# Performance work log

Measured on AMD Instinct MI355X. Metric: run time of the kernel, lower is better.

## Reference

```python
import jax, jax.numpy as jnp
import numpy as np
from jax import lax

D_MODEL = 1024
D_STATE = 16
D_CONV = 4
EXPAND = 2
D_INNER = EXPAND * D_MODEL           # 2048 (mamba inner)
DT_RANK = (D_MODEL + 15) // 16       # 64
D_FF = 4 * D_MODEL                   # 4096 (SwiGLU hidden)
EPS = 1e-5
B, L = 2, 2048


def setup_inputs() -> dict:
    key = jax.random.key(0)
    ks = jax.random.split(key, 16)
    s = 0.02
    inp = {
        'x': jax.random.normal(ks[0], (B, L, D_MODEL), jnp.float32),
        'norm1_w': jnp.ones((D_MODEL,), jnp.float32),
        'norm2_w': jnp.ones((D_MODEL,), jnp.float32),
        # Mamba params (torch Linear convention: y = x @ W.T)
        'in_proj_w': s * jax.random.normal(ks[1], (2 * D_INNER, D_MODEL), jnp.float32),
        'conv_w': s * jax.random.normal(ks[2], (D_INNER, 1, D_CONV), jnp.float32),
        'conv_b': jnp.zeros((D_INNER,), jnp.float32),
        'x_proj_w': s * jax.random.normal(ks[3], (DT_RANK + 2 * D_STATE, D_INNER), jnp.float32),
        'dt_proj_w': s * jax.random.normal(ks[4], (D_INNER, DT_RANK), jnp.float32),
        'dt_proj_b': jax.random.uniform(ks[5], (D_INNER,), jnp.float32, -4.0, -2.0),
        'A_log': jnp.log(jnp.broadcast_to(jnp.arange(1, D_STATE + 1, dtype=jnp.float32), (D_INNER, D_STATE))),
        'D': jnp.ones((D_INNER,), jnp.float32),
        'out_proj_w': s * jax.random.normal(ks[6], (D_MODEL, D_INNER), jnp.float32),
        # SwiGLU MLP
        'w1': s * jax.random.normal(ks[7], (D_FF, D_MODEL), jnp.float32),
        'w2': s * jax.random.normal(ks[8], (D_FF, D_MODEL), jnp.float32),
        'w3': s * jax.random.normal(ks[9], (D_MODEL, D_FF), jnp.float32),
    }
    return inp


def _rmsnorm(x, w, eps=EPS):
    return x * lax.rsqrt(jnp.mean(x * x, axis=-1, keepdims=True) + eps) * w


def _mamba(x, in_proj_w, conv_w, conv_b, x_proj_w, dt_proj_w, dt_proj_b, A_log, Dp, out_proj_w):
    # x: (B, L, d_model)
    xz = x @ in_proj_w.T                       # (B, L, 2*d_inner)
    u, z = jnp.split(xz, 2, axis=-1)           # each (B, L, d_inner)
    # causal depthwise conv1d over time
    u_nch = u.transpose(0, 2, 1)               # (B, d_inner, L)
    u_conv = lax.conv_general_dilated(
        u_nch, conv_w, window_strides=(1,), padding=[(D_CONV - 1, 0)],
        dimension_numbers=('NCH', 'OIH', 'NCH'), feature_group_count=D_INNER)
    u_conv = u_conv + conv_b[None, :, None]
    u_act = jax.nn.silu(u_conv.transpose(0, 2, 1))   # (B, L, d_inner)
    # input-dependent dt, B, C
    proj = u_act @ x_proj_w.T                  # (B, L, dt_rank + 2*d_state)
    dt_r, Bm, Cm = jnp.split(proj, [DT_RANK, DT_RANK + D_STATE], axis=-1)
    dt = jax.nn.softplus(dt_r @ dt_proj_w.T + dt_proj_b)   # (B, L, d_inner)
    A = -jnp.exp(A_log)                        # (d_inner, d_state)
    dA = jnp.exp(jnp.einsum('bld,dn->bldn', dt, A))
    dBu = jnp.einsum('bld,bln,bld->bldn', dt, Bm, u_act)
    def step(h, inputs):
        dA_t, dBu_t = inputs                   # (B, d_inner, d_state)
        h = dA_t * h + dBu_t
        return h, h
    h0 = jnp.zeros((x.shape[0], D_INNER, D_STATE), x.dtype)
    _, hs = lax.scan(step, h0, (dA.transpose(1, 0, 2, 3), dBu.transpose(1, 0, 2, 3)))
    y = jnp.einsum('lbdn,bln->bld', hs, Cm) + u_act * Dp   # (B, L, d_inner)
    y = y * jax.nn.silu(z)
    return y @ out_proj_w.T                    # (B, L, d_model)


def reference(x, norm1_w, norm2_w, in_proj_w, conv_w, conv_b, x_proj_w,
              dt_proj_w, dt_proj_b, A_log, D, out_proj_w, w1, w2, w3):
    # residual + RMSNorm + Mamba (dropout = eval-mode identity)
    h = x + _mamba(_rmsnorm(x, norm1_w), in_proj_w, conv_w, conv_b,
                   x_proj_w, dt_proj_w, dt_proj_b, A_log, D, out_proj_w)
    # residual + RMSNorm + SwiGLU MLP
    xn = _rmsnorm(h, norm2_w)
    mlp = (jax.nn.silu(xn @ w1.T) * (xn @ w2.T)) @ w3.T
    return h + mlp
```

## Files before the change

kernel.cpp:

```cpp
#include <hip/hip_runtime.h>
#include <hip/hip_bf16.h>

#define TOKS 4096
#define DM   1024
#define DI   2048
#define DST  16
#define DTR  64
#define DFF  4096
#define PROJ_LD 128

#define NC    32
#define CHUNK 64

typedef __bf16 bf16x8 __attribute__((ext_vector_type(8)));
typedef float  f32x4  __attribute__((ext_vector_type(4)));

__device__ __forceinline__ __bf16 f2bf(float f) {
  union { float f; unsigned u; } v; v.f = f;
  unsigned r = v.u + 0x7fffu + ((v.u >> 16) & 1u);
  union { unsigned short s; __bf16 b; } o; o.s = (unsigned short)(r >> 16);
  return o.b;
}
__device__ __forceinline__ float siluf(float x) { return x / (1.f + __expf(-x)); }
__device__ __forceinline__ float softplusf(float x) { return x > 20.f ? x : log1pf(__expf(x)); }

__device__ __forceinline__ void gl2lds16(const void* g, void* l) {
  __builtin_amdgcn_global_load_lds((const __attribute__((address_space(1))) void*)g,
                                   (__attribute__((address_space(3))) void*)l, 16, 0, 0);
}

struct CvtArgs {
  const float* src[5];
  __bf16*      dst[5];
  int nblk[6];
};

__global__ __launch_bounds__(256) void cvt_bf16_kernel(CvtArgs a) {
  int blk = blockIdx.x;
  int seg = 0;
#pragma unroll
  for (int s = 1; s < 5; s++) if (blk >= a.nblk[s]) seg = s;
  size_t base = (size_t)(blk - a.nblk[seg]) * 2048 + threadIdx.x * 8;
  const float* src = a.src[seg] + base;
  __bf16*      dst = a.dst[seg] + base;
  float4 v0 = *(const float4*)src;
  float4 v1 = *(const float4*)(src + 4);
  union { __bf16 b[8]; uint4 u; } t;
  t.b[0]=f2bf(v0.x); t.b[1]=f2bf(v0.y); t.b[2]=f2bf(v0.z); t.b[3]=f2bf(v0.w);
  t.b[4]=f2bf(v1.x); t.b[5]=f2bf(v1.y); t.b[6]=f2bf(v1.z); t.b[7]=f2bf(v1.w);
  *(uint4*)dst = t.u;
}

__global__ __launch_bounds__(256) void cvt_w12_kernel(const float* __restrict__ w1,
                                                      const float* __restrict__ w2,
                                                      __bf16* __restrict__ dst) {
  int blk = blockIdx.x;
  int isw2 = blk >> 11;
  int b = blk & 2047;
  int r = b * 2 + (threadIdx.x >> 7);
  int col = (threadIdx.x & 127) * 8;
  const float* src = (isw2 ? w2 : w1) + (size_t)r * DM + col;
  int dr = (r >> 4) * 32 + (r & 15) + isw2 * 16;
  float4 v0 = *(const float4*)src;
  float4 v1 = *(const float4*)(src + 4);
  union { __bf16 b[8]; uint4 u; } t;
  t.b[0]=f2bf(v0.x); t.b[1]=f2bf(v0.y); t.b[2]=f2bf(v0.z); t.b[3]=f2bf(v0.w);
  t.b[4]=f2bf(v1.x); t.b[5]=f2bf(v1.y); t.b[6]=f2bf(v1.z); t.b[7]=f2bf(v1.w);
  *(uint4*)&dst[(size_t)dr * DM + col] = t.u;
}

__global__ __launch_bounds__(256) void rmsnorm_kernel(const float* __restrict__ x,
                                                      const float* __restrict__ w,
                                                      __bf16* __restrict__ out) {
  int row = blockIdx.x;
  const float* xr = x + (size_t)row * DM;
  float4 v = ((const float4*)xr)[threadIdx.x];
  float ss = v.x*v.x + v.y*v.y + v.z*v.z + v.w*v.w;
#pragma unroll
  for (int o = 32; o > 0; o >>= 1) ss += __shfl_xor(ss, o);
  __shared__ float sred[4];
  if ((threadIdx.x & 63) == 0) sred[threadIdx.x >> 6] = ss;
  __syncthreads();
  float tot = sred[0] + sred[1] + sred[2] + sred[3];
  float scale = rsqrtf(tot * (1.f / DM) + 1e-5f);
  float4 wv = ((const float4*)w)[threadIdx.x];
  union { __bf16 b[4]; ushort4 u; } o;
  o.b[0] = f2bf(v.x * scale * wv.x);
  o.b[1] = f2bf(v.y * scale * wv.y);
  o.b[2] = f2bf(v.z * scale * wv.z);
  o.b[3] = f2bf(v.w * scale * wv.w);
  *(ushort4*)&out[(size_t)row * DM + threadIdx.x * 4] = o.u;
}

template<int BM, int EPI, int SWAP, int KK, int Z, int LDA, int LDB, int LDC>
__global__ __launch_bounds__(256, BM == 128 ? 1 : 2) void gemm2(
    const void* __restrict__ Ap, const __bf16* __restrict__ Bp,
    void* __restrict__ Cp, const void* __restrict__ auxp)
{
  constexpr int FM = BM / 32;
  constexpr int AI = BM / 64;
  constexpr int kPer = KK / Z;
  __shared__ __bf16 sA[2][BM * 32];
  __shared__ __bf16 sB[2][128 * 32];
  const int tid  = threadIdx.x;
  const int wave = tid >> 6, lane = tid & 63;
  const int bm = SWAP ? blockIdx.x : blockIdx.y;
  const int bn = SWAP ? blockIdx.y : blockIdx.x;
  const int m0 = bm * BM, n0 = bn * 128;
  const int wr = wave >> 1, wc = wave & 1;
  const int frow = lane & 15, fq = lane >> 4;

  f32x4 acc[FM][4] = {};

  const int kBeg = (Z > 1) ? blockIdx.z * kPer : 0;
  const int kEnd = kBeg + kPer;

  const int lrow = lane >> 2;
  const int lcol = (lane & 3) * 8;

  auto stage = [&](int kt, int buf) {
#pragma unroll
    for (int q = 0; q < AI; q++) {
      int idx = wave * AI + q;
      gl2lds16((const __bf16*)Ap + (size_t)(m0 + idx * 16 + lrow) * LDA + kt + lcol,
               &sA[buf][idx * 512]);
    }
#pragma unroll
    for (int q = 0; q < 2; q++) {
      int idx = wave * 2 + q;
      gl2lds16(Bp + (size_t)(n0 + idx * 16 + lrow) * LDB + kt + lcol,
               &sB[buf][idx * 512]);
    }
  };

  stage(kBeg, 0);
  int cur = 0;
  for (int kt = kBeg; kt < kEnd; kt += 32) {
    __syncthreads();

    bf16x8 afr[FM], bfr[4];
#pragma unroll
    for (int i = 0; i < FM; i++)
      afr[i] = *(const bf16x8*)&sA[cur][(wr * (BM/2) + i * 16 + frow) * 32 + fq * 8];
#pragma unroll
    for (int j = 0; j < 4; j++)
      bfr[j] = *(const bf16x8*)&sB[cur][(wc * 64 + j * 16 + frow) * 32 + fq * 8];

    if (kt + 32 < kEnd) stage(kt + 32, cur ^ 1);

#pragma unroll
    for (int i = 0; i < FM; i++)
#pragma unroll
      for (int j = 0; j < 4; j++)
        acc[i][j] = __builtin_amdgcn_mfma_f32_16x16x32_bf16(afr[i], bfr[j], acc[i][j], 0, 0, 0);
    cur ^= 1;
  }

  const float* auxf = (const float*)auxp;
#pragma unroll
  for (int i = 0; i < FM; i++) {
    int gr = m0 + wr * (BM/2) + i * 16 + fq * 4;
#pragma unroll
    for (int j = 0; j < 4; j++) {
      int gc = n0 + wc * 64 + j * 16 + frow;
#pragma unroll
      for (int r = 0; r < 4; r++) {
        float v = acc[i][j][r];
        size_t off = (size_t)(gr + r) * LDC + gc;
        if (EPI == 1) ((__bf16*)Cp)[off] = f2bf(v);
        else if (EPI == 2) ((__bf16*)Cp)[off] = f2bf(softplusf(v + auxf[gc]));
        else if (EPI == 3) ((float*)Cp)[off] = v + auxf[off];
        else if (EPI == 7)
          ((float*)Cp)[(size_t)blockIdx.z * (TOKS * PROJ_LD) + off] = v;
      }
    }
  }
}

template<int KK, int LDA, int LDB, int LDC>
__global__ __launch_bounds__(256, 2) void gemm2d(
    const __bf16* __restrict__ Ap, const __bf16* __restrict__ Bp,
    float* __restrict__ Cp, const float* __restrict__ auxp)
{
  constexpr int NSTEP = KK / 32;
  static_assert(NSTEP % 4 == 0 && NSTEP >= 8, "KK must be mult of 128");
  __shared__ alignas(16) char S2[49152];
  const int tid  = threadIdx.x;
  const int wave = tid >> 6, lane = tid & 63;
  const int m0 = blockIdx.x * 64, n0 = blockIdx.y * 128;
  const int wr = wave >> 1, wc = wave & 1;
  const int frow = lane & 15, fq = lane >> 4;
  const int lrow = lane >> 2, lcol = (lane & 3) * 8;

  f32x4 acc[2][4] = {};

  const unsigned s2 = (unsigned)(size_t)(__attribute__((address_space(3))) char*)S2;
  const unsigned aAddr = s2 + (unsigned)((wr * 32 + frow) * 64 + fq * 16);
  const unsigned bAddr = s2 + 16384u + (unsigned)((wc * 64 + frow) * 64 + fq * 16);

  auto stage = [&](int tile, int buf) {
    gl2lds16(Ap + (size_t)(m0 + wave * 16 + lrow) * LDA + tile * 32 + lcol,
             S2 + buf * 4096 + wave * 1024);
#pragma unroll
    for (int q = 0; q < 2; q++) {
      int idx = wave * 2 + q;
      gl2lds16(Bp + (size_t)(n0 + idx * 16 + lrow) * LDB + tile * 32 + lcol,
               S2 + 16384 + buf * 8192 + idx * 1024);
    }
  };

#define D_SB() __builtin_amdgcn_sched_barrier(0)
#define D_DSR(dst, addr, OFF)                                                  \
    asm volatile("ds_read_b128 %0, %1 offset:" OFF : "=v"(dst) : "v"(addr))
#define D_STEP(t, B, OA0, OA1, OB0, OB1, OB2, OB3)                             \
  do {                                                                         \
    if ((t) + 3 < NSTEP) stage((t) + 3, ((B) + 3) & 3);                        \
    D_SB();                                                                    \
    if ((t) + 3 < NSTEP)      asm volatile("s_waitcnt vmcnt(9)");              \
    else if ((t) + 2 < NSTEP) asm volatile("s_waitcnt vmcnt(6)");              \
    else if ((t) + 1 < NSTEP) asm volatile("s_waitcnt vmcnt(3)");              \
    else                      asm volatile("s_waitcnt vmcnt(0)");              \
    D_SB();                                                                    \
    __builtin_amdgcn_s_barrier();              \
    D_SB();                                                                    \
    f32x4 ta0, ta1, tb0, tb1, tb2, tb3;                                        \
    D_DSR(ta0, aAddr, OA0); D_DSR(ta1, aAddr, OA1);                            \
    D_DSR(tb0, bAddr, OB0); D_DSR(tb1, bAddr, OB1);                            \
    D_DSR(tb2, bAddr, OB2); D_DSR(tb3, bAddr, OB3);                            \
    asm volatile("s_waitcnt lgkmcnt(0)");                                      \
    D_SB();                                                                    \
    __builtin_amdgcn_s_barrier();           \
    D_SB();                                                                    \
    bf16x8 a0 = __builtin_bit_cast(bf16x8, ta0);                               \
    bf16x8 a1 = __builtin_bit_cast(bf16x8, ta1);                               \
    bf16x8 b0 = __builtin_bit_cast(bf16x8, tb0);                               \
    bf16x8 b1 = __builtin_bit_cast(bf16x8, tb1);                               \
    bf16x8 b2 = __builtin_bit_cast(bf16x8, tb2);                               \
    bf16x8 b3 = __builtin_bit_cast(bf16x8, tb3);                               \
    acc[0][0] = __builtin_amdgcn_mfma_f32_16x16x32_bf16(a0, b0, acc[0][0], 0, 0, 0); \
    acc[0][1] = __builtin_amdgcn_mfma_f32_16x16x32_bf16(a0, b1, acc[0][1], 0, 0, 0); \
    acc[0][2] = __builtin_amdgcn_mfma_f32_16x16x32_bf16(a0, b2, acc[0][2], 0, 0, 0); \
    acc[0][3] = __builtin_amdgcn_mfma_f32_16x16x32_bf16(a0, b3, acc[0][3], 0, 0, 0); \
    acc[1][0] = __builtin_amdgcn_mfma_f32_16x16x32_bf16(a1, b0, acc[1][0], 0, 0, 0); \
    acc[1][1] = __builtin_amdgcn_mfma_f32_16x16x32_bf16(a1, b1, acc[1][1], 0, 0, 0); \
    acc[1][2] = __builtin_amdgcn_mfma_f32_16x16x32_bf16(a1, b2, acc[1][2], 0, 0, 0); \
    acc[1][3] = __builtin_amdgcn_mfma_f32_16x16x32_bf16(a1, b3, acc[1][3], 0, 0, 0); \
  } while (0)

  stage(0, 0); stage(1, 1); stage(2, 2);
  for (int t = 0; t < NSTEP; t += 4) {
    D_STEP(t + 0, 0, "0",     "1024",  "0",     "1024",  "2048",  "3072");
    D_STEP(t + 1, 1, "4096",  "5120",  "8192",  "9216",  "10240", "11264");
    D_STEP(t + 2, 2, "8192",  "9216",  "16384", "17408", "18432", "19456");
    D_STEP(t + 3, 3, "12288", "13312", "24576", "25600", "26624", "27648");
  }
#undef D_STEP
#undef D_DSR
#undef D_SB

#pragma unroll
  for (int i = 0; i < 2; i++) {
    int gr = m0 + wr * 32 + i * 16 + fq * 4;
#pragma unroll
    for (int j = 0; j < 4; j++) {
      int gc = n0 + wc * 64 + j * 16 + frow;
#pragma unroll
      for (int r = 0; r < 4; r++) {
        size_t off = (size_t)(gr + r) * LDC + gc;
        Cp[off] = acc[i][j][r] + auxp[off];
      }
    }
  }
}

template<int EPI, int KK, int LDA, int LDB, int LDC, int GX>
__global__ __launch_bounds__(512, 2) void gemm8(
    const __bf16* __restrict__ Ap, const __bf16* __restrict__ Bp,
    void* __restrict__ Cp)
{
  constexpr int NT = KK / 64;
  static_assert(NT % 2 == 0 && NT >= 4, "KK must be a multiple of 128");
  __shared__ alignas(16) char S[131072];

  const int tid  = threadIdx.x;
  const int wid  = tid >> 6, lane = tid & 63;
  const int wr   = wid >> 2, wc = wid & 3;
  const int bid = blockIdx.y * (GX * 8) + blockIdx.x;
  const int xcd = bid & 7, idx = bid >> 3;
  const int m0 = (idx / GX) * 256;
  const int n0 = (xcd * GX + (idx % GX)) * 256;
  const int frow = lane & 15, fq = lane >> 4;
  const int cbyt = (fq * 16) ^ (((lane >> 3) & 1) << 5);
  const int srow = lane >> 2;
  const int skin = ((lane & 3) * 8) ^ (((lane >> 5) & 1) << 4);

  const unsigned sbase = (unsigned)(size_t)(__attribute__((address_space(3))) char*)S;
  const unsigned abase = sbase + (unsigned)((wr * 64 + frow) * 64 + cbyt);
  const unsigned bbase = sbase + 32768u + (unsigned)((wc * 32 + frow) * 64 + cbyt);

  f32x4 acc[2][2][4][2] = {};
  bf16x8 fA[4][2], fB0[2][2], fB1[2][2];

#define G8_SB() __builtin_amdgcn_sched_barrier(0)
#define G8_BAR() do { G8_SB(); __builtin_amdgcn_s_barrier(); G8_SB(); } while (0)
#define G8_LGKM0() do { asm volatile("s_waitcnt lgkmcnt(0)"); G8_SB(); } while (0)
#define G8_THROT() asm volatile("s_waitcnt lgkmcnt(8)")
#define G8_WAIT6() asm volatile("s_waitcnt vmcnt(6)")
#define G8_WAIT0() asm volatile("s_waitcnt vmcnt(0)")
#define G8_DSR(dst, addr, OFF)                                                 \
    asm volatile("ds_read_b128 %0, %1 offset:" OFF : "=v"(dst) : "v"(addr))

#define G8_STAGE(buf, ab, h, tile) do {                                        \
    if ((tile) < NT) {                                                         \
      const __bf16* gb = (ab) ? Bp : Ap;                                       \
      const int ld = (ab) ? LDB : LDA;                                         \
      const int r0 = ((ab) ? n0 : m0) + (h) * 128;                             \
      _Pragma("unroll")                                                        \
      for (int q = 0; q < 2; q++) {                                            \
        int p = wid * 2 + q, kk = p >> 3, r16 = p & 7;                         \
        const __bf16* src = gb + (size_t)(r0 + r16 * 16 + srow) * ld           \
                            + (tile) * 64 + kk * 32 + skin;                    \
        char* dst = S + (((buf) * 4 + (ab) * 2 + kk) << 14)                    \
                    + ((h) * 128 + r16 * 16) * 64;                             \
        gl2lds16(src, dst);                                                    \
      }                                                                        \
    }                                                                          \
  } while (0)

#define G8_READ_A(buf, mh) do {                                                \
    unsigned a_ = abase + (buf) * 65536u + (mh) * 8192u;                       \
    f32x4 t0,t1,t2,t3,t4,t5,t6,t7;                                             \
    G8_DSR(t0, a_, "0");     G8_DSR(t1, a_, "1024");                           \
    G8_DSR(t2, a_, "2048");  G8_DSR(t3, a_, "3072");                           \
    G8_DSR(t4, a_, "16384"); G8_DSR(t5, a_, "17408");                          \
    G8_DSR(t6, a_, "18432"); G8_DSR(t7, a_, "19456");                          \
    fA[0][0]=__builtin_bit_cast(bf16x8,t0); fA[1][0]=__builtin_bit_cast(bf16x8,t1); \
    fA[2][0]=__builtin_bit_cast(bf16x8,t2); fA[3][0]=__builtin_bit_cast(bf16x8,t3); \
    fA[0][1]=__builtin_bit_cast(bf16x8,t4); fA[1][1]=__builtin_bit_cast(bf16x8,t5); \
    fA[2][1]=__builtin_bit_cast(bf16x8,t6); fA[3][1]=__builtin_bit_cast(bf16x8,t7); \
  } while (0)

#define G8_READ_B(buf, nh, FB) do {                                            \
    unsigned b_ = bbase + (buf) * 65536u + (nh) * 8192u;                       \
    f32x4 t0,t1,t2,t3;                                                         \
    G8_DSR(t0, b_, "0");     G8_DSR(t1, b_, "1024");                           \
    G8_DSR(t2, b_, "16384"); G8_DSR(t3, b_, "17408");                          \
    FB[0][0]=__builtin_bit_cast(bf16x8,t0); FB[1][0]=__builtin_bit_cast(bf16x8,t1); \
    FB[0][1]=__builtin_bit_cast(bf16x8,t2); FB[1][1]=__builtin_bit_cast(bf16x8,t3); \
  } while (0)

#define G8_MFMA(mh, nh, FB) do {                                               \
    __builtin_amdgcn_s_setprio(1);                                             \
    _Pragma("unroll")                                                          \
    for (int kk = 0; kk < 2; kk++)                                             \
      _Pragma("unroll")                                                        \
      for (int fi = 0; fi < 4; fi++)                                           \
        _Pragma("unroll")                                                      \
        for (int fj = 0; fj < 2; fj++)                                         \
          acc[mh][nh][fi][fj] = __builtin_amdgcn_mfma_f32_16x16x32_bf16(       \
              fA[fi][kk], FB[fj][kk], acc[mh][nh][fi][fj], 0, 0, 0);           \
    __builtin_amdgcn_s_setprio(0);                                             \
    G8_SB();                                                                   \
  } while (0)

  G8_STAGE(0, 0, 0, 0); G8_STAGE(0, 1, 1, 0); G8_STAGE(0, 0, 1, 0); G8_STAGE(0, 1, 0, 0);
  G8_STAGE(1, 0, 0, 1); G8_STAGE(1, 1, 1, 1); G8_STAGE(1, 0, 1, 1);
  G8_SB();
  G8_WAIT6();
  G8_BAR();

  for (int it = 0; it < NT / 2; ++it) {
    const int t1 = 2 * it + 1, t2 = 2 * it + 2, t3 = 2 * it + 3;
    const bool last = (it == NT / 2 - 1);
    G8_READ_A(0, 0); G8_READ_B(0, 0, fB0);
    G8_STAGE(1, 1, 0, t1);
    G8_SB(); G8_THROT();
    G8_BAR();
    G8_LGKM0();
    G8_MFMA(0, 0, fB0);
    G8_BAR();
    G8_READ_B(0, 1, fB1);
    G8_STAGE(0, 0, 0, t2);
    G8_SB();
    G8_BAR();
    G8_LGKM0();
    G8_MFMA(0, 1, fB1);
    G8_BAR();
    G8_READ_A(0, 1);
    G8_STAGE(0, 1, 1, t2);
    G8_SB();
    G8_BAR();
    G8_LGKM0();
    G8_MFMA(1, 1, fB1);
    G8_BAR();
    G8_STAGE(0, 0, 1, t2);
    G8_SB();
    if (last) G8_WAIT0(); else G8_WAIT6();
    G8_BAR();
    G8_MFMA(1, 0, fB0);
    G8_BAR();
    G8_READ_A(1, 0); G8_READ_B(1, 0, fB0);
    G8_STAGE(0, 1, 0, t2);
    G8_SB(); G8_THROT();
    G8_BAR();
    G8_LGKM0();
    G8_MFMA(0, 0, fB0);
    G8_BAR();
    G8_READ_B(1, 1, fB1);
    G8_STAGE(1, 0, 0, t3);
    G8_SB();
    G8_BAR();
    G8_LGKM0();
    G8_MFMA(0, 1, fB1);
    G8_BAR();
    G8_READ_A(1, 1);
    G8_STAGE(1, 1, 1, t3);
    G8_SB();
    G8_BAR();
    G8_LGKM0();
    G8_MFMA(1, 1, fB1);
    G8_BAR();
    G8_STAGE(1, 0, 1, t3);
    G8_SB();
    if (!last) G8_WAIT6();
    G8_BAR();
    G8_MFMA(1, 0, fB0);
    G8_BAR();
  }

#undef G8_STAGE
#undef G8_READ_A
#undef G8_READ_B
#undef G8_MFMA
#undef G8_BAR
#undef G8_SB
#undef G8_LGKM0
#undef G8_THROT
#undef G8_WAIT6
#undef G8_WAIT0
#undef G8_DSR

#pragma unroll
  for (int mh = 0; mh < 2; mh++)
#pragma unroll
    for (int nh = 0; nh < 2; nh++)
#pragma unroll
      for (int fi = 0; fi < 4; fi++) {
        int gr = m0 + mh * 128 + wr * 64 + fi * 16 + fq * 4;
        if constexpr (EPI == 1) {
#pragma unroll
          for (int fj = 0; fj < 2; fj++) {
            int gc = n0 + nh * 128 + wc * 32 + fj * 16 + frow;
#pragma unroll
            for (int r = 0; r < 4; r++)
              ((__bf16*)Cp)[(size_t)(gr + r) * LDC + gc] = f2bf(acc[mh][nh][fi][fj][r]);
          }
        } else {
          int col = ((n0 + nh * 128 + wc * 32) >> 1) + frow;
#pragma unroll
          for (int r = 0; r < 4; r++) {
            float g = acc[mh][nh][fi][0][r];
            float v = acc[mh][nh][fi][1][r];
            ((__bf16*)Cp)[(size_t)(gr + r) * LDC + col] = f2bf(siluf(g) * v);
          }
        }
      }
}

__global__ __launch_bounds__(256) void xp_reduce_kernel(const float* __restrict__ part,
                                                        float* __restrict__ proj,
                                                        __bf16* __restrict__ projb) {
  int i = blockIdx.x * 256 + threadIdx.x;
  float4 s = ((const float4*)part)[i];
#pragma unroll
  for (int z = 1; z < 8; z++) {
    float4 v = ((const float4*)(part + (size_t)z * TOKS * PROJ_LD))[i];
    s.x += v.x; s.y += v.y; s.z += v.z; s.w += v.w;
  }
  ((float4*)proj)[i] = s;
  int c4 = i & 31;
  if (c4 < 16) {
    int tok = i >> 5;
    union { __bf16 b[4]; ushort4 u; } t;
    t.b[0]=f2bf(s.x); t.b[1]=f2bf(s.y); t.b[2]=f2bf(s.z); t.b[3]=f2bf(s.w);
    *(ushort4*)&projb[(size_t)tok * 64 + c4 * 4] = t.u;
  }
}

__global__ __launch_bounds__(256) void conv_silu_kernel(const __bf16* __restrict__ xz,
                                                        const float* __restrict__ cw,
                                                        const float* __restrict__ cb,
                                                        __bf16* __restrict__ uact) {
  int idx = blockIdx.x * 256 + threadIdx.x;
  int d8  = (idx & 255) * 8;
  int tok = idx >> 8;
  int l   = tok & 2047;
  const __bf16* up = xz + (size_t)tok * (2 * DI) + d8;
  bf16x8 u0 = {}, u1 = {}, u2 = {}, u3;
  if (l >= 3) u0 = *(const bf16x8*)(up - 3 * (2 * DI));
  if (l >= 2) u1 = *(const bf16x8*)(up - 2 * (2 * DI));
  if (l >= 1) u2 = *(const bf16x8*)(up - 1 * (2 * DI));
  u3 = *(const bf16x8*)up;
  float4 cb0 = *(const float4*)(cb + d8);
  float4 cb1 = *(const float4*)(cb + d8 + 4);
  float cbv[8] = {cb0.x, cb0.y, cb0.z, cb0.w, cb1.x, cb1.y, cb1.z, cb1.w};
  union { __bf16 b[8]; uint4 u; } res;
#pragma unroll
  for (int j = 0; j < 8; j++) {
    float4 wv = *(const float4*)(cw + (size_t)(d8 + j) * 4);
    float acc = cbv[j];
    acc += wv.x * (float)u0[j];
    acc += wv.y * (float)u1[j];
    acc += wv.z * (float)u2[j];
    acc += wv.w * (float)u3[j];
    res.b[j] = f2bf(siluf(acc));
  }
  *(uint4*)&uact[(size_t)tok * DI + d8] = res.u;
}

__global__ __launch_bounds__(64) void scan_pass1(const __bf16* __restrict__ dt,
                                                 const __bf16* __restrict__ uact,
                                                 const float* __restrict__ proj,
                                                 const float* __restrict__ A_log,
                                                 float* __restrict__ aprod,
                                                 float* __restrict__ hend) {
  int lane = threadIdx.x;
  int d = blockIdx.x * 64 + lane;
  int c = blockIdx.y, b = blockIdx.z;
  float An[16], h[16], ap[16];
  {
    const float4* a4 = (const float4*)(A_log + (size_t)d * 16);
#pragma unroll
    for (int q = 0; q < 4; q++) {
      float4 v = a4[q];
      An[q*4+0] = -__expf(v.x); An[q*4+1] = -__expf(v.y);
      An[q*4+2] = -__expf(v.z); An[q*4+3] = -__expf(v.w);
    }
  }
#pragma unroll
  for (int n = 0; n < 16; n++) { h[n] = 0.f; ap[n] = 1.f; }

  size_t tok = (size_t)b * 2048 + (size_t)c * CHUNK;
  const __bf16* dtp = dt   + tok * DI + d;
  const __bf16* up  = uact + tok * DI + d;
  const float*  pp  = proj + tok * PROJ_LD;

  for (int t = 0; t < CHUNK; t++) {
    float dtv = (float)*dtp;
    float uv  = (float)*up;
    const float4* b4 = (const float4*)(pp + 64);
    float Bv[16];
#pragma unroll
    for (int q = 0; q < 4; q++) {
      float4 v = b4[q];
      Bv[q*4+0]=v.x; Bv[q*4+1]=v.y; Bv[q*4+2]=v.z; Bv[q*4+3]=v.w;
    }
    float du = dtv * uv;
#pragma unroll
    for (int n = 0; n < 16; n++) {
      float dA = __expf(dtv * An[n]);
      ap[n] *= dA;
      h[n] = fmaf(dA, h[n], du * Bv[n]);
    }
    dtp += DI; up += DI; pp += PROJ_LD;
  }

  size_t off = ((size_t)(b * NC + c) * DI + d) * 16;
#pragma unroll
  for (int q = 0; q < 4; q++) {
    *(float4*)(hend  + off + q*4) = make_float4(h[q*4+0],  h[q*4+1],  h[q*4+2],  h[q*4+3]);
    *(float4*)(aprod + off + q*4) = make_float4(ap[q*4+0], ap[q*4+1], ap[q*4+2], ap[q*4+3]);
  }
}

__global__ __launch_bounds__(256) void scan_pass2(const float* __restrict__ aprod,
                                                  const float* __restrict__ hend,
                                                  float* __restrict__ hstart) {
  int idx = blockIdx.x * 256 + threadIdx.x;
  int b  = idx >> 13;
  int r4 = idx & 8191;
  float4 H = make_float4(0.f, 0.f, 0.f, 0.f);
  for (int c = 0; c < NC; c++) {
    size_t off = (size_t)(b * NC + c) * (DI * 16 / 4) + r4;
    ((float4*)hstart)[off] = H;
    float4 a = ((const float4*)aprod)[off];
    float4 e = ((const float4*)hend)[off];
    H.x = fmaf(a.x, H.x, e.x);
    H.y = fmaf(a.y, H.y, e.y);
    H.z = fmaf(a.z, H.z, e.z);
    H.w = fmaf(a.w, H.w, e.w);
  }
}

__global__ __launch_bounds__(64) void scan_pass3(const __bf16* __restrict__ dt,
                                                 const __bf16* __restrict__ uact,
                                                 const float* __restrict__ proj,
                                                 const __bf16* __restrict__ xz,
                                                 const float* __restrict__ A_log,
                                                 const float* __restrict__ Dp,
                                                 const float* __restrict__ hstart,
                                                 __bf16* __restrict__ y) {
  int lane = threadIdx.x;
  int d = blockIdx.x * 64 + lane;
  int c = blockIdx.y, b = blockIdx.z;
  float An[16], h[16];
  {
    const float4* a4 = (const float4*)(A_log + (size_t)d * 16);
#pragma unroll
    for (int q = 0; q < 4; q++) {
      float4 v = a4[q];
      An[q*4+0] = -__expf(v.x); An[q*4+1] = -__expf(v.y);
      An[q*4+2] = -__expf(v.z); An[q*4+3] = -__expf(v.w);
    }
  }
  {
    size_t off = ((size_t)(b * NC + c) * DI + d) * 16;
#pragma unroll
    for (int q = 0; q < 4; q++) {
      float4 v = *(const float4*)(hstart + off + q*4);
      h[q*4+0]=v.x; h[q*4+1]=v.y; h[q*4+2]=v.z; h[q*4+3]=v.w;
    }
  }
  float Dd = Dp[d];

  size_t tok = (size_t)b * 2048 + (size_t)c * CHUNK;
  const __bf16* dtp = dt   + tok * DI + d;
  const __bf16* up  = uact + tok * DI + d;
  const float*  pp  = proj + tok * PROJ_LD;
  const __bf16* zp  = xz   + tok * (2 * DI) + DI + d;
  __bf16*       yp  = y    + tok * DI + d;

  for (int t = 0; t < CHUNK; t++) {
    float dtv = (float)*dtp;
    float uv  = (float)*up;
    float zv  = (float)*zp;
    const float4* b4 = (const float4*)(pp + 64);
    float Bv[16], Cv[16];
#pragma unroll
    for (int q = 0; q < 4; q++) {
      float4 v = b4[q];
      Bv[q*4+0]=v.x; Bv[q*4+1]=v.y; Bv[q*4+2]=v.z; Bv[q*4+3]=v.w;
      float4 w = b4[q + 4];
      Cv[q*4+0]=w.x; Cv[q*4+1]=w.y; Cv[q*4+2]=w.z; Cv[q*4+3]=w.w;
    }
    float du = dtv * uv;
    float p = 0.f;
#pragma unroll
    for (int n = 0; n < 16; n++) {
      float dA = __expf(dtv * An[n]);
      h[n] = fmaf(dA, h[n], du * Bv[n]);
      p = fmaf(h[n], Cv[n], p);
    }
    *yp = f2bf((p + Dd * uv) * siluf(zv));
    dtp += DI; up += DI; pp += PROJ_LD; zp += 2 * DI; yp += DI;
  }
}

extern "C" void kernel_launch(void* const* d_in, const int* in_sizes, int n_in,
                              void* d_out, int out_size, void* d_ws, size_t ws_size,
                              hipStream_t stream) {
  const float* x        = (const float*)d_in[0];
  const float* n1w      = (const float*)d_in[1];
  const float* n2w      = (const float*)d_in[2];
  const float* in_projw = (const float*)d_in[3];
  const float* conv_w   = (const float*)d_in[4];
  const float* conv_b   = (const float*)d_in[5];
  const float* x_projw  = (const float*)d_in[6];
  const float* dt_projw = (const float*)d_in[7];
  const float* dt_projb = (const float*)d_in[8];
  const float* A_log    = (const float*)d_in[9];
  const float* Dp       = (const float*)d_in[10];
  const float* out_projw= (const float*)d_in[11];
  const float* w1       = (const float*)d_in[12];
  const float* w2       = (const float*)d_in[13];
  const float* w3       = (const float*)d_in[14];
  float* out = (float*)d_out;

  char* ws = (char*)d_ws;
  __bf16* xz   = (__bf16*)(ws + 0);
  __bf16* uact = (__bf16*)(ws + 33554432);
  float*  proj = (float*) (ws + 50331648);
  __bf16* dt   = (__bf16*)(ws + 52428800);
  __bf16* yb   = (__bf16*)(ws + 85983232);
  float*  xpp  = (float*) (ws + 85983232);
  float*  h    = (float*) (ws + 102760448);
  __bf16* xn   = (__bf16*)(ws + 119537664);
  __bf16* hid  = xz;
  __bf16* projb = (__bf16*)(ws + 102760448);
  float* aprod  = (float*)(ws + 102760448);
  float* hend   = (float*)(ws + 111149056);
  float* hstart = (float*)(ws + 119537664);
  char* wb = ws + 127926272;
  __bf16* b_in  = (__bf16*)(wb);
  __bf16* b_xp  = (__bf16*)(wb + 8388608);
  __bf16* b_dtp = (__bf16*)(wb + 8912896);
  __bf16* b_out = (__bf16*)(wb + 9175040);
  __bf16* b_w12 = (__bf16*)(wb + 13369344);
  __bf16* b_w3  = (__bf16*)(wb + 30146560);

  hipMemsetAsync(b_xp, 0, 128 * 2048 * sizeof(__bf16), stream);

  CvtArgs ca;
  const float* srcs[5] = {in_projw, x_projw, dt_projw, out_projw, w3};
  __bf16* dsts[5]      = {b_in, b_xp, b_dtp, b_out, b_w3};
  int counts[5] = {4096*1024, 96*2048, 2048*64, 1024*2048, 1024*4096};
  int acc = 0;
  for (int i = 0; i < 5; i++) { ca.src[i] = srcs[i]; ca.dst[i] = dsts[i]; ca.nblk[i] = acc; acc += counts[i] / 2048; }
  ca.nblk[5] = acc;
  cvt_bf16_kernel<<<acc, 256, 0, stream>>>(ca);
  cvt_w12_kernel<<<4096, 256, 0, stream>>>(w1, w2, b_w12);

  dim3 blk(256);
  rmsnorm_kernel<<<TOKS, 256, 0, stream>>>(x, n1w, xn);
  gemm8<1, 1024, DM, DM, 4096, 2><<<dim3(16, 16), 512, 0, stream>>>(xn, b_in, xz);
  conv_silu_kernel<<<(TOKS*DI/8)/256, 256, 0, stream>>>(xz, conv_w, conv_b, uact);
  gemm2<64,7,0, 2048,8, DI,DI,PROJ_LD><<<dim3(1,64,8), blk, 0, stream>>>(uact, b_xp, xpp, nullptr);
  xp_reduce_kernel<<<512, 256, 0, stream>>>(xpp, proj, projb);
  gemm2<128,2,0, 64,1, 64,DTR,DI><<<dim3(16,32,1), blk, 0, stream>>>(projb, b_dtp, dt, dt_projb);
  scan_pass1<<<dim3(DI/64, NC, 2), 64, 0, stream>>>(dt, uact, proj, A_log, aprod, hend);
  scan_pass2<<<64, 256, 0, stream>>>(aprod, hend, hstart);
  scan_pass3<<<dim3(DI/64, NC, 2), 64, 0, stream>>>(dt, uact, proj, xz, A_log, Dp, hstart, yb);
  gemm2d<2048, DI, DI, DM><<<dim3(64, 8), blk, 0, stream>>>(yb, b_out, h, x);
  rmsnorm_kernel<<<TOKS, 256, 0, stream>>>(h, n2w, xn);
  gemm8<6, 1024, DM, DM, DFF, 4><<<dim3(32, 16), 512, 0, stream>>>(xn, b_w12, hid);
  gemm2d<4096, DFF, DFF, DM><<<dim3(64, 8), blk, 0, stream>>>(hid, b_w3, out, h);

  (void)in_sizes; (void)n_in; (void)out_size; (void)ws_size;
}
```

Baseline: 509.5 us.

## Prefetch next-step operands in scan kernels, interleave LDS waits with MFMAs, reuse gemm2d for x_proj

The scan pass1/pass2/pass3 loops now load the next timestep's dt, u, z and B/C values (or the next chunk's aprod/hend) into registers before computing the current step, which hides global-load latency behind the serial recurrence. In gemm2d, the full lgkmcnt(0) wait before all MFMAs is replaced by staged lgkmcnt waits, so each column's MFMAs can issue as soon as its LDS read lands. The last column's MFMAs move after the second barrier. gemm2d also gains an epilogue selector and a split-K z dimension, so the x_proj GEMM now uses it in place of gemm2 with 64 M-tiles and 8 K-splits. The costs are extra registers for the prefetched values and a different tiling for the small x_proj GEMM.

```diff
diff --git a/kernel.cpp b/kernel.cpp
--- a/kernel.cpp
+++ b/kernel.cpp
@@ -177,13 +177,14 @@
   }
 }
 
-template<int KK, int LDA, int LDB, int LDC>
+template<int EPI, int KK, int Z, int LDA, int LDB, int LDC>
 __global__ __launch_bounds__(256, 2) void gemm2d(
     const __bf16* __restrict__ Ap, const __bf16* __restrict__ Bp,
     float* __restrict__ Cp, const float* __restrict__ auxp)
 {
-  constexpr int NSTEP = KK / 32;
-  static_assert(NSTEP % 4 == 0 && NSTEP >= 8, "KK must be mult of 128");
+  constexpr int kPer = KK / Z;
+  constexpr int NSTEP = kPer / 32;
+  static_assert(NSTEP % 4 == 0 && NSTEP >= 8, "kPer must be mult of 128, >=256");
   __shared__ alignas(16) char S2[49152];
   const int tid  = threadIdx.x;
   const int wave = tid >> 6, lane = tid & 63;
@@ -191,6 +192,7 @@
   const int wr = wave >> 1, wc = wave & 1;
   const int frow = lane & 15, fq = lane >> 4;
   const int lrow = lane >> 2, lcol = (lane & 3) * 8;
+  const int kBeg = (Z > 1) ? blockIdx.z * kPer : 0;
 
   f32x4 acc[2][4] = {};
 
@@ -198,13 +200,14 @@
   const unsigned aAddr = s2 + (unsigned)((wr * 32 + frow) * 64 + fq * 16);
   const unsigned bAddr = s2 + 16384u + (unsigned)((wc * 64 + frow) * 64 + fq * 16);
 
-  auto stage = [&](int tile, int buf) {
-    gl2lds16(Ap + (size_t)(m0 + wave * 16 + lrow) * LDA + tile * 32 + lcol,
+  auto stage = [&](int t, int buf) {
+    int kt = kBeg + t * 32;
+    gl2lds16(Ap + (size_t)(m0 + wave * 16 + lrow) * LDA + kt + lcol,
              S2 + buf * 4096 + wave * 1024);
 #pragma unroll
     for (int q = 0; q < 2; q++) {
       int idx = wave * 2 + q;
-      gl2lds16(Bp + (size_t)(n0 + idx * 16 + lrow) * LDB + tile * 32 + lcol,
+      gl2lds16(Bp + (size_t)(n0 + idx * 16 + lrow) * LDB + kt + lcol,
                S2 + 16384 + buf * 8192 + idx * 1024);
     }
   };
@@ -212,6 +215,10 @@
 #define D_SB() __builtin_amdgcn_sched_barrier(0)
 #define D_DSR(dst, addr, OFF)                                                  \
     asm volatile("ds_read_b128 %0, %1 offset:" OFF : "=v"(dst) : "v"(addr))
+#define D_MM(i, j, A, Bv)                                                      \
+    acc[i][j] = __builtin_amdgcn_mfma_f32_16x16x32_bf16(                       \
+        __builtin_bit_cast(bf16x8, A), __builtin_bit_cast(bf16x8, Bv),         \
+        acc[i][j], 0, 0, 0)
 #define D_STEP(t, B, OA0, OA1, OB0, OB1, OB2, OB3)                             \
   do {                                                                         \
     if ((t) + 3 < NSTEP) stage((t) + 3, ((B) + 3) & 3);                        \
@@ -227,24 +234,17 @@
     D_DSR(ta0, aAddr, OA0); D_DSR(ta1, aAddr, OA1);                            \
     D_DSR(tb0, bAddr, OB0); D_DSR(tb1, bAddr, OB1);                            \
     D_DSR(tb2, bAddr, OB2); D_DSR(tb3, bAddr, OB3);                            \
-    asm volatile("s_waitcnt lgkmcnt(0)");                                      \
     D_SB();                                                                    \
+    asm volatile("s_waitcnt lgkmcnt(3)"); D_SB();                              \
+    D_MM(0, 0, ta0, tb0); D_MM(1, 0, ta1, tb0);                                \
+    asm volatile("s_waitcnt lgkmcnt(2)"); D_SB();                              \
+    D_MM(0, 1, ta0, tb1); D_MM(1, 1, ta1, tb1);                                \
+    asm volatile("s_waitcnt lgkmcnt(1)"); D_SB();                              \
+    D_MM(0, 2, ta0, tb2); D_MM(1, 2, ta1, tb2);                                \
+    asm volatile("s_waitcnt lgkmcnt(0)"); D_SB();                              \
     __builtin_amdgcn_s_barrier();           \
     D_SB();                                                                    \
-    bf16x8 a0 = __builtin_bit_cast(bf16x8, ta0);                               \
-    bf16x8 a1 = __builtin_bit_cast(bf16x8, ta1);                               \
-    bf16x8 b0 = __builtin_bit_cast(bf16x8, tb0);                               \
-    bf16x8 b1 = __builtin_bit_cast(bf16x8, tb1);                               \
-    bf16x8 b2 = __builtin_bit_cast(bf16x8, tb2);                               \
-    bf16x8 b3 = __builtin_bit_cast(bf16x8, tb3);                               \
-    acc[0][0] = __builtin_amdgcn_mfma_f32_16x16x32_bf16(a0, b0, acc[0][0], 0, 0, 0); \
-    acc[0][1] = __builtin_amdgcn_mfma_f32_16x16x32_bf16(a0, b1, acc[0][1], 0, 0, 0); \
-    acc[0][2] = __builtin_amdgcn_mfma_f32_16x16x32_bf16(a0, b2, acc[0][2], 0, 0, 0); \
-    acc[0][3] = __builtin_amdgcn_mfma_f32_16x16x32_bf16(a0, b3, acc[0][3], 0, 0, 0); \
-    acc[1][0] = __builtin_amdgcn_mfma_f32_16x16x32_bf16(a1, b0, acc[1][0], 0, 0, 0); \
-    acc[1][1] = __builtin_amdgcn_mfma_f32_16x16x32_bf16(a1, b1, acc[1][1], 0, 0, 0); \
-    acc[1][2] = __builtin_amdgcn_mfma_f32_16x16x32_bf16(a1, b2, acc[1][2], 0, 0, 0); \
-    acc[1][3] = __builtin_amdgcn_mfma_f32_16x16x32_bf16(a1, b3, acc[1][3], 0, 0, 0); \
+    D_MM(0, 3, ta0, tb3); D_MM(1, 3, ta1, tb3);                                \
   } while (0)
 
   stage(0, 0); stage(1, 1); stage(2, 2);
@@ -255,6 +255,7 @@
     D_STEP(t + 3, 3, "12288", "13312", "24576", "25600", "26624", "27648");
   }
 #undef D_STEP
+#undef D_MM
 #undef D_DSR
 #undef D_SB
 
@@ -267,7 +268,9 @@
 #pragma unroll
       for (int r = 0; r < 4; r++) {
         size_t off = (size_t)(gr + r) * LDC + gc;
-        Cp[off] = acc[i][j][r] + auxp[off];
+        if (EPI == 3) Cp[off] = acc[i][j][r] + auxp[off];
+        else if (EPI == 7)
+          Cp[(size_t)blockIdx.z * (TOKS * PROJ_LD) + off] = acc[i][j][r];
       }
     }
   }
@@ -545,16 +548,22 @@
   const __bf16* up  = uact + tok * DI + d;
   const float*  pp  = proj + tok * PROJ_LD;
 
+  float dtv = (float)*dtp;
+  float uv  = (float)*up;
+  float4 B0, B1, B2, B3;
+  { const float4* b4 = (const float4*)(pp + 64); B0=b4[0]; B1=b4[1]; B2=b4[2]; B3=b4[3]; }
+
   for (int t = 0; t < CHUNK; t++) {
-    float dtv = (float)*dtp;
-    float uv  = (float)*up;
-    const float4* b4 = (const float4*)(pp + 64);
-    float Bv[16];
-#pragma unroll
-    for (int q = 0; q < 4; q++) {
-      float4 v = b4[q];
-      Bv[q*4+0]=v.x; Bv[q*4+1]=v.y; Bv[q*4+2]=v.z; Bv[q*4+3]=v.w;
-    }
+    float dtv_n = 0.f, uv_n = 0.f;
+    float4 N0 = B0, N1 = B1, N2 = B2, N3 = B3;
+    if (t + 1 < CHUNK) {
+      const float4* nb = (const float4*)(pp + PROJ_LD + 64);
+      dtv_n = (float)dtp[DI];
+      uv_n  = (float)up[DI];
+      N0 = nb[0]; N1 = nb[1]; N2 = nb[2]; N3 = nb[3];
+    }
+    float Bv[16] = {B0.x,B0.y,B0.z,B0.w, B1.x,B1.y,B1.z,B1.w,
+                    B2.x,B2.y,B2.z,B2.w, B3.x,B3.y,B3.z,B3.w};
     float du = dtv * uv;
 #pragma unroll
     for (int n = 0; n < 16; n++) {
@@ -562,6 +571,7 @@
       ap[n] *= dA;
       h[n] = fmaf(dA, h[n], du * Bv[n]);
     }
+    dtv = dtv_n; uv = uv_n; B0 = N0; B1 = N1; B2 = N2; B3 = N3;
     dtp += DI; up += DI; pp += PROJ_LD;
   }
 
@@ -580,15 +590,23 @@
   int b  = idx >> 13;
   int r4 = idx & 8191;
   float4 H = make_float4(0.f, 0.f, 0.f, 0.f);
+  size_t off = (size_t)(b * NC) * (DI * 16 / 4) + r4;
+  float4 a = ((const float4*)aprod)[off];
+  float4 e = ((const float4*)hend)[off];
   for (int c = 0; c < NC; c++) {
-    size_t off = (size_t)(b * NC + c) * (DI * 16 / 4) + r4;
+    float4 an = a, en = e;
+    if (c + 1 < NC) {
+      size_t noff = off + (DI * 16 / 4);
+      an = ((const float4*)aprod)[noff];
+      en = ((const float4*)hend)[noff];
+    }
     ((float4*)hstart)[off] = H;
-    float4 a = ((const float4*)aprod)[off];
-    float4 e = ((const float4*)hend)[off];
     H.x = fmaf(a.x, H.x, e.x);
     H.y = fmaf(a.y, H.y, e.y);
     H.z = fmaf(a.z, H.z, e.z);
     H.w = fmaf(a.w, H.w, e.w);
+    a = an; e = en;
+    off += (DI * 16 / 4);
   }
 }
 
@@ -630,19 +648,27 @@
   const __bf16* zp  = xz   + tok * (2 * DI) + DI + d;
   __bf16*       yp  = y    + tok * DI + d;
 
+  float dtv = (float)*dtp;
+  float uv  = (float)*up;
+  float zv  = (float)*zp;
+  float4 P0,P1,P2,P3,P4,P5,P6,P7;
+  { const float4* b4 = (const float4*)(pp + 64);
+    P0=b4[0];P1=b4[1];P2=b4[2];P3=b4[3];P4=b4[4];P5=b4[5];P6=b4[6];P7=b4[7]; }
+
   for (int t = 0; t < CHUNK; t++) {
-    float dtv = (float)*dtp;
-    float uv  = (float)*up;
-    float zv  = (float)*zp;
-    const float4* b4 = (const float4*)(pp + 64);
-    float Bv[16], Cv[16];
-#pragma unroll
-    for (int q = 0; q < 4; q++) {
-      float4 v = b4[q];
-      Bv[q*4+0]=v.x; Bv[q*4+1]=v.y; Bv[q*4+2]=v.z; Bv[q*4+3]=v.w;
-      float4 w = b4[q + 4];
-      Cv[q*4+0]=w.x; Cv[q*4+1]=w.y; Cv[q*4+2]=w.z; Cv[q*4+3]=w.w;
-    }
+    float dtv_n = 0.f, uv_n = 0.f, zv_n = 0.f;
+    float4 Q0=P0,Q1=P1,Q2=P2,Q3=P3,Q4=P4,Q5=P5,Q6=P6,Q7=P7;
+    if (t + 1 < CHUNK) {
+      const float4* nb = (const float4*)(pp + PROJ_LD + 64);
+      dtv_n = (float)dtp[DI];
+      uv_n  = (float)up[DI];
+      zv_n  = (float)zp[2 * DI];
+      Q0=nb[0];Q1=nb[1];Q2=nb[2];Q3=nb[3];Q4=nb[4];Q5=nb[5];Q6=nb[6];Q7=nb[7];
+    }
+    float Bv[16] = {P0.x,P0.y,P0.z,P0.w, P1.x,P1.y,P1.z,P1.w,
+                    P2.x,P2.y,P2.z,P2.w, P3.x,P3.y,P3.z,P3.w};
+    float Cv[16] = {P4.x,P4.y,P4.z,P4.w, P5.x,P5.y,P5.z,P5.w,
+                    P6.x,P6.y,P6.z,P6.w, P7.x,P7.y,P7.z,P7.w};
     float du = dtv * uv;
     float p = 0.f;
 #pragma unroll
@@ -652,6 +678,8 @@
       p = fmaf(h[n], Cv[n], p);
     }
     *yp = f2bf((p + Dd * uv) * siluf(zv));
+    dtv = dtv_n; uv = uv_n; zv = zv_n;
+    P0=Q0;P1=Q1;P2=Q2;P3=Q3;P4=Q4;P5=Q5;P6=Q6;P7=Q7;
     dtp += DI; up += DI; pp += PROJ_LD; zp += 2 * DI; yp += DI;
   }
 }
@@ -714,16 +742,16 @@
   rmsnorm_kernel<<<TOKS, 256, 0, stream>>>(x, n1w, xn);
   gemm8<1, 1024, DM, DM, 4096, 2><<<dim3(16, 16), 512, 0, stream>>>(xn, b_in, xz);
   conv_silu_kernel<<<(TOKS*DI/8)/256, 256, 0, stream>>>(xz, conv_w, conv_b, uact);
-  gemm2<64,7,0, 2048,8, DI,DI,PROJ_LD><<<dim3(1,64,8), blk, 0, stream>>>(uact, b_xp, xpp, nullptr);
+  gemm2d<7, 2048, 8, DI, DI, PROJ_LD><<<dim3(64, 1, 8), blk, 0, stream>>>(uact, b_xp, xpp, nullptr);
   xp_reduce_kernel<<<512, 256, 0, stream>>>(xpp, proj, projb);
   gemm2<128,2,0, 64,1, 64,DTR,DI><<<dim3(16,32,1), blk, 0, stream>>>(projb, b_dtp, dt, dt_projb);
   scan_pass1<<<dim3(DI/64, NC, 2), 64, 0, stream>>>(dt, uact, proj, A_log, aprod, hend);
   scan_pass2<<<64, 256, 0, stream>>>(aprod, hend, hstart);
   scan_pass3<<<dim3(DI/64, NC, 2), 64, 0, stream>>>(dt, uact, proj, xz, A_log, Dp, hstart, yb);
-  gemm2d<2048, DI, DI, DM><<<dim3(64, 8), blk, 0, stream>>>(yb, b_out, h, x);
+  gemm2d<3, 2048, 1, DI, DI, DM><<<dim3(64, 8), blk, 0, stream>>>(yb, b_out, h, x);
   rmsnorm_kernel<<<TOKS, 256, 0, stream>>>(h, n2w, xn);
   gemm8<6, 1024, DM, DM, DFF, 4><<<dim3(32, 16), 512, 0, stream>>>(xn, b_w12, hid);
-  gemm2d<4096, DFF, DFF, DM><<<dim3(64, 8), blk, 0, stream>>>(hid, b_w3, out, h);
+  gemm2d<3, 4096, 1, DFF, DFF, DM><<<dim3(64, 8), blk, 0, stream>>>(hid, b_w3, out, h);
 
   (void)in_sizes; (void)n_in; (void)out_size; (void)ws_size;
 }
```

After: 505.6 us. No clear change (-0.8%).
